# Kernel tuning notes

Hardware: AMD Instinct MI355X
Metric: run time of the kernel (lower is better)

Reference implementation:

```python
import jax, jax.numpy as jnp
import numpy as np

NUM_HEADS = 12

def setup_inputs() -> dict:
    key = jax.random.key(0)
    ks = jax.random.split(key, 6)
    B, N, C, T = 1, 4096, 768, 16
    return {
        "x": jax.random.normal(ks[0], (B, N, C), dtype=jnp.float32),
        "templates": jax.random.normal(ks[1], (T, 3 * C, C), dtype=jnp.float32) * 0.02,
        "coeffs": jax.random.normal(ks[2], (2, T, 1), dtype=jnp.float32),
        "qkv_bias": jnp.zeros((3 * C,), dtype=jnp.float32),
        "proj_w": jax.random.normal(ks[3], (C, C), dtype=jnp.float32) * 0.02,
        "proj_b": jnp.zeros((C,), dtype=jnp.float32),
    }

def reference(x, templates, coeffs, qkv_bias, proj_w, proj_b):
    B, N, C = x.shape
    H = NUM_HEADS
    hd = C // H
    scale = hd ** -0.5
    # template bank: each of num_cf coefficient sets builds a (3C, C) weight; average them
    num_cf = coeffs.shape[0]
    qkv_w = jnp.einsum('kt,toi->oi', coeffs[:, :, 0], templates) / num_cf  # (3C, C)
    qkv = x @ qkv_w.T + qkv_bias                                          # (B, N, 3C)
    qkv = qkv.reshape(B, N, 3, H, hd).transpose(2, 0, 3, 1, 4)            # (3, B, H, N, hd)
    q, k, v = qkv[0], qkv[1], qkv[2]
    attn = jax.nn.softmax(jnp.einsum('bhnd,bhmd->bhnm', q, k) * scale, axis=-1)
    out = jnp.einsum('bhnm,bhmd->bhnd', attn, v)                          # (B, H, N, hd)
    out = out.transpose(0, 2, 1, 3).reshape(B, N, C)
    return out @ proj_w.T + proj_b
```

## Files before the change

kernel.cpp:

```cpp
#include <hip/hip_runtime.h>
#include <stdint.h>

#define N_SEQ 4096
#define C_DIM 768
#define HEADS 12
#define HD    64
#define OI    (2304*768)

typedef __attribute__((ext_vector_type(8))) short short8;
typedef __attribute__((ext_vector_type(4))) float f32x4;
typedef __attribute__((ext_vector_type(16))) float f32x16;

__device__ __forceinline__ short f2bf(float f) {
  union { float f; unsigned u; } v; v.f = f;
  unsigned r = v.u + 0x7FFF + ((v.u >> 16) & 1);
  return (short)(r >> 16);
}
__device__ __forceinline__ short f2bf_trunc(float f) {
  union { float f; unsigned u; } v; v.f = f;
  return (short)(v.u >> 16);
}

__global__ __launch_bounds__(256) void prep_qkvw(const float* __restrict__ tmpl,
                                                 const float* __restrict__ coeffs,
                                                 short* __restrict__ w_bf) {
  __shared__ float c[16];
  if (threadIdx.x < 16)
    c[threadIdx.x] = 0.5f * (coeffs[threadIdx.x] + coeffs[16 + threadIdx.x]);
  __syncthreads();
  int idx = blockIdx.x * 256 + threadIdx.x;
  int base = idx * 4;
  if (base >= OI) return;
  float ax = 0.f, ay = 0.f, az = 0.f, aw = 0.f;
#pragma unroll
  for (int t = 0; t < 16; ++t) {
    float4 v = *(const float4*)(tmpl + (size_t)t * OI + base);
    float ct = c[t];
    ax = fmaf(ct, v.x, ax); ay = fmaf(ct, v.y, ay);
    az = fmaf(ct, v.z, az); aw = fmaf(ct, v.w, aw);
  }
  short4 o = make_short4(f2bf(ax), f2bf(ay), f2bf(az), f2bf(aw));
  *(short4*)(w_bf + base) = o;
}

__global__ __launch_bounds__(256) void cvt_bf16(const float* __restrict__ src,
                                                short* __restrict__ dst, int n4) {
  int i = blockIdx.x * 256 + threadIdx.x;
  if (i >= n4) return;
  float4 v = ((const float4*)src)[i];
  ((short4*)dst)[i] = make_short4(f2bf(v.x), f2bf(v.y), f2bf(v.z), f2bf(v.w));
}

#define GST 40
#define QSCALE 0.1803368801111204f
__global__ __launch_bounds__(256) void gemm_qkv(const short* __restrict__ A,
                                                const short* __restrict__ B,
                                                const float* __restrict__ bias,
                                                short* __restrict__ qkv_out) {
  __shared__ short As[128 * GST];
  __shared__ short Bs[128 * GST];
  int tid = threadIdx.x;
  int wave = tid >> 6, lane = tid & 63, g = lane >> 4, l15 = lane & 15;
  int wm = (wave >> 1) * 64, wn = (wave & 1) * 64;
  size_t mblk = (size_t)blockIdx.x * 128;
  size_t nblk = (size_t)blockIdx.y * 128;

  f32x4 acc[4][4];
#pragma unroll
  for (int mi = 0; mi < 4; ++mi)
#pragma unroll
    for (int ni = 0; ni < 4; ++ni)
#pragma unroll
      for (int r = 0; r < 4; ++r) acc[mi][ni][r] = 0.f;

  int row0 = tid >> 2;
  int c8   = (tid & 3) * 8;

  for (int k0 = 0; k0 < 768; k0 += 32) {
    short8 a0 = *(const short8*)(A + (mblk + row0) * 768 + k0 + c8);
    short8 a1 = *(const short8*)(A + (mblk + row0 + 64) * 768 + k0 + c8);
    short8 b0 = *(const short8*)(B + (nblk + row0) * 768 + k0 + c8);
    short8 b1 = *(const short8*)(B + (nblk + row0 + 64) * 768 + k0 + c8);
    __syncthreads();
    *(short8*)(As + row0 * GST + c8) = a0;
    *(short8*)(As + (row0 + 64) * GST + c8) = a1;
    *(short8*)(Bs + row0 * GST + c8) = b0;
    *(short8*)(Bs + (row0 + 64) * GST + c8) = b1;
    __syncthreads();
    short8 af[4], bfr[4];
#pragma unroll
    for (int mi = 0; mi < 4; ++mi)
      af[mi] = *(const short8*)(As + (wm + mi * 16 + l15) * GST + g * 8);
#pragma unroll
    for (int ni = 0; ni < 4; ++ni)
      bfr[ni] = *(const short8*)(Bs + (wn + ni * 16 + l15) * GST + g * 8);
#pragma unroll
    for (int mi = 0; mi < 4; ++mi)
#pragma unroll
      for (int ni = 0; ni < 4; ++ni)
        acc[mi][ni] = __builtin_amdgcn_mfma_f32_16x16x32_bf16(af[mi], bfr[ni], acc[mi][ni], 0, 0, 0);
  }

#pragma unroll
  for (int ni = 0; ni < 4; ++ni) {
    int col = (int)nblk + wn + ni * 16 + l15;
    int which = col / 768;
    int rem = col - which * 768;
    int h = rem >> 6, d = rem & 63;
    float bcol = bias[col];
    if (which == 2) {
      short* vbase = qkv_out + (size_t)2 * HEADS * N_SEQ * HD
                   + ((size_t)h * HD + d) * N_SEQ;
#pragma unroll
      for (int mi = 0; mi < 4; ++mi) {
        int rowb = (int)mblk + wm + mi * 16 + g * 4;
        short4 o;
        o.x = f2bf(acc[mi][ni][0] + bcol);
        o.y = f2bf(acc[mi][ni][1] + bcol);
        o.z = f2bf(acc[mi][ni][2] + bcol);
        o.w = f2bf(acc[mi][ni][3] + bcol);
        *(short4*)(vbase + rowb) = o;
      }
    } else {
      float sc = (which == 0) ? QSCALE : 1.0f;
      short* dst = qkv_out + ((size_t)which * HEADS + h) * N_SEQ * HD + d;
#pragma unroll
      for (int mi = 0; mi < 4; ++mi) {
        int rowb = (int)mblk + wm + mi * 16 + g * 4;
#pragma unroll
        for (int r = 0; r < 4; ++r)
          dst[(size_t)(rowb + r) * HD] = f2bf((acc[mi][ni][r] + bcol) * sc);
      }
    }
  }
}

__global__ __launch_bounds__(256) void gemm_proj(const short* __restrict__ A,
                                                 const short* __restrict__ B,
                                                 const float* __restrict__ bias,
                                                 float* __restrict__ C) {
  __shared__ short As[64 * GST];
  __shared__ short Bs[64 * GST];
  int tid = threadIdx.x;
  int wave = tid >> 6, lane = tid & 63, g = lane >> 4, l15 = lane & 15;
  int wm = (wave >> 1) * 32, wn = (wave & 1) * 32;
  size_t mblk = (size_t)blockIdx.x * 64;
  size_t nblk = (size_t)blockIdx.y * 64;

  f32x4 acc[2][2];
#pragma unroll
  for (int mi = 0; mi < 2; ++mi)
#pragma unroll
    for (int ni = 0; ni < 2; ++ni)
#pragma unroll
      for (int r = 0; r < 4; ++r) acc[mi][ni][r] = 0.f;

  int row0 = tid >> 2;
  int c8   = (tid & 3) * 8;

  for (int k0 = 0; k0 < 768; k0 += 32) {
    short8 a0 = *(const short8*)(A + (mblk + row0) * 768 + k0 + c8);
    short8 b0 = *(const short8*)(B + (nblk + row0) * 768 + k0 + c8);
    __syncthreads();
    *(short8*)(As + row0 * GST + c8) = a0;
    *(short8*)(Bs + row0 * GST + c8) = b0;
    __syncthreads();
    short8 af[2], bfr[2];
#pragma unroll
    for (int mi = 0; mi < 2; ++mi)
      af[mi] = *(const short8*)(As + (wm + mi * 16 + l15) * GST + g * 8);
#pragma unroll
    for (int ni = 0; ni < 2; ++ni)
      bfr[ni] = *(const short8*)(Bs + (wn + ni * 16 + l15) * GST + g * 8);
#pragma unroll
    for (int mi = 0; mi < 2; ++mi)
#pragma unroll
      for (int ni = 0; ni < 2; ++ni)
        acc[mi][ni] = __builtin_amdgcn_mfma_f32_16x16x32_bf16(af[mi], bfr[ni], acc[mi][ni], 0, 0, 0);
  }

#pragma unroll
  for (int ni = 0; ni < 2; ++ni) {
    int col = (int)nblk + wn + ni * 16 + l15;
    float bcol = bias[col];
#pragma unroll
    for (int mi = 0; mi < 2; ++mi) {
      int rowb = (int)mblk + wm + mi * 16 + g * 4;
#pragma unroll
      for (int r = 0; r < 4; ++r)
        C[(size_t)(rowb + r) * 768 + col] = acc[mi][ni][r] + bcol;
    }
  }
}

#define PST 68
__global__ __launch_bounds__(128) void attn_fa(const short* __restrict__ qkv_buf,
                                               short* __restrict__ out_bf) {
  __shared__ short Ks[64 * PST];
  __shared__ short Vt[64 * PST];
  __shared__ short Ps[2 * 32 * PST];
  __shared__ float ls[64];
  int h = blockIdx.y;
  int q0 = blockIdx.x * 64;
  int tid = threadIdx.x, wave = tid >> 6, lane = tid & 63;
  int q5 = lane & 31, h5 = lane >> 5;
  const short* qh  = qkv_buf + (size_t)(0 * HEADS + h) * N_SEQ * HD;
  const short* kh  = qkv_buf + (size_t)(1 * HEADS + h) * N_SEQ * HD;
  const short* vth = qkv_buf + (size_t)2 * HEADS * N_SEQ * HD + (size_t)h * HD * N_SEQ;

  short8 qf[4];
#pragma unroll
  for (int c = 0; c < 4; ++c)
    qf[c] = *(const short8*)(qh + (size_t)(q0 + wave * 32 + q5) * HD + c * 16 + h5 * 8);

  f32x16 o_acc[2];
#pragma unroll
  for (int dt = 0; dt < 2; ++dt)
#pragma unroll
    for (int r = 0; r < 16; ++r) o_acc[dt][r] = 0.f;
  float l_r = 0.f;

  int srow = tid >> 1;
  int shalf = (tid & 1) * 32;

  short8 kr[4], vr[4];
#pragma unroll
  for (int i = 0; i < 4; ++i) {
    kr[i] = *(const short8*)(kh + (size_t)srow * HD + shalf + 8 * i);
    vr[i] = *(const short8*)(vth + (size_t)srow * N_SEQ + shalf + 8 * i);
  }

  short* pw = Ps + wave * 32 * PST;

  for (int t0 = 0; t0 < N_SEQ; t0 += 64) {
    __syncthreads();
#pragma unroll
    for (int i = 0; i < 4; ++i) {
      *(short8*)(Ks + srow * PST + shalf + 8 * i) = kr[i];
      *(short8*)(Vt + srow * PST + shalf + 8 * i) = vr[i];
    }
    __syncthreads();

    if (t0 + 64 < N_SEQ) {
      int t1 = t0 + 64;
#pragma unroll
      for (int i = 0; i < 4; ++i) {
        kr[i] = *(const short8*)(kh + (size_t)(t1 + srow) * HD + shalf + 8 * i);
        vr[i] = *(const short8*)(vth + (size_t)srow * N_SEQ + t1 + shalf + 8 * i);
      }
    }

    f32x16 st[2];
#pragma unroll
    for (int kt = 0; kt < 2; ++kt)
#pragma unroll
      for (int r = 0; r < 16; ++r) st[kt][r] = 0.f;
#pragma unroll
    for (int c = 0; c < 4; ++c)
#pragma unroll
      for (int kt = 0; kt < 2; ++kt) {
        short8 kf = *(const short8*)(Ks + (kt * 32 + q5) * PST + c * 16 + h5 * 8);
        st[kt] = __builtin_amdgcn_mfma_f32_32x32x16_bf16(kf, qf[c], st[kt], 0, 0, 0);
      }

#pragma unroll
    for (int kt = 0; kt < 2; ++kt)
#pragma unroll
      for (int cc = 0; cc < 4; ++cc) {
        float p0 = __builtin_amdgcn_exp2f(st[kt][cc * 4 + 0]);
        float p1 = __builtin_amdgcn_exp2f(st[kt][cc * 4 + 1]);
        float p2 = __builtin_amdgcn_exp2f(st[kt][cc * 4 + 2]);
        float p3 = __builtin_amdgcn_exp2f(st[kt][cc * 4 + 3]);
        l_r += (p0 + p1) + (p2 + p3);
        short4 o = make_short4(f2bf_trunc(p0), f2bf_trunc(p1), f2bf_trunc(p2), f2bf_trunc(p3));
        *(short4*)(pw + q5 * PST + kt * 32 + cc * 8 + h5 * 4) = o;
      }

#pragma unroll
    for (int c = 0; c < 4; ++c) {
      short8 pf = *(const short8*)(pw + q5 * PST + c * 16 + h5 * 8);
#pragma unroll
      for (int dt = 0; dt < 2; ++dt) {
        short8 vf = *(const short8*)(Vt + (dt * 32 + q5) * PST + c * 16 + h5 * 8);
        o_acc[dt] = __builtin_amdgcn_mfma_f32_32x32x16_bf16(pf, vf, o_acc[dt], 0, 0, 0);
      }
    }
  }

  l_r += __shfl_xor(l_r, 32);
  if (h5 == 0) ls[wave * 32 + q5] = 1.0f / l_r;
  __syncthreads();

#pragma unroll
  for (int cc = 0; cc < 4; ++cc)
#pragma unroll
    for (int rr = 0; rr < 4; ++rr) {
      int qloc = rr + 8 * cc + 4 * h5;
      float inv = ls[wave * 32 + qloc];
      int qrow = q0 + wave * 32 + qloc;
#pragma unroll
      for (int dt = 0; dt < 2; ++dt)
        out_bf[(size_t)qrow * C_DIM + h * HD + dt * 32 + q5] =
            f2bf(o_acc[dt][cc * 4 + rr] * inv);
    }
}

extern "C" void kernel_launch(void* const* d_in, const int* in_sizes, int n_in,
                              void* d_out, int out_size, void* d_ws, size_t ws_size,
                              hipStream_t stream) {
  const float* x        = (const float*)d_in[0];
  const float* tmpl     = (const float*)d_in[1];
  const float* coeffs   = (const float*)d_in[2];
  const float* qkv_bias = (const float*)d_in[3];
  const float* proj_w   = (const float*)d_in[4];
  const float* proj_b   = (const float*)d_in[5];
  float* out = (float*)d_out;
  char* ws = (char*)d_ws;

  short* w_bf    = (short*)(ws);
  short* x_bf    = (short*)(ws + 3538944);
  short* pw_bf   = (short*)(ws + 9830400);
  short* qkvb    = (short*)(ws + 11010048);
  short* attn_bf = (short*)(ws + 29884416);

  prep_qkvw<<<1728, 256, 0, stream>>>(tmpl, coeffs, w_bf);
  cvt_bf16<<<3072, 256, 0, stream>>>(x, x_bf, 786432);
  cvt_bf16<<<576, 256, 0, stream>>>(proj_w, pw_bf, 147456);

  dim3 g1(32, 18);
  gemm_qkv<<<g1, 256, 0, stream>>>(x_bf, w_bf, qkv_bias, qkvb);

  dim3 ga(64, 12);
  attn_fa<<<ga, 128, 0, stream>>>(qkvb, attn_bf);

  dim3 g2(64, 12);
  gemm_proj<<<g2, 256, 0, stream>>>(attn_bf, pw_bf, proj_b, out);
}
```

Before: 349.3 us.

## Split attention KV range in two with partial outputs and a reduce kernel

Attention now splits each head's key range into two halves, doubling the grid to 1536 blocks, with a swizzled block index to spread heads across XCDs. Each half writes unnormalized fp32 partial outputs and row sums, and a new reduce kernel combines them, normalizes and converts to bf16. K fragments are now read straight from global memory instead of being staged in LDS, and launch bounds request higher occupancy. The cost is extra fp32 partial traffic, one more launch, and uncached-by-LDS K loads; the output buffer is reused as scratch for one partial.

New measurement: 372.1 us. +6.5%, slower.

```diff
diff --git a/kernel.cpp b/kernel.cpp
--- a/kernel.cpp
+++ b/kernel.cpp
@@ -194,16 +194,22 @@
 }
 
 #define PST 68
-__global__ __launch_bounds__(128) void attn_fa(const short* __restrict__ qkv_buf,
-                                               short* __restrict__ out_bf) {
-  __shared__ short Ks[64 * PST];
+__global__ __launch_bounds__(128, 3) void attn_fa(const short* __restrict__ qkv_buf,
+                                                  float* __restrict__ op0,
+                                                  float* __restrict__ op1,
+                                                  float* __restrict__ lp) {
   __shared__ short Vt[64 * PST];
   __shared__ short Ps[2 * 32 * PST];
-  __shared__ float ls[64];
-  int h = blockIdx.y;
-  int q0 = blockIdx.x * 64;
+  int bid = blockIdx.x;
+  int j = (bid & 7) * 192 + (bid >> 3);
+  int h = j >> 7;
+  int rj = j & 127;
+  int half = rj >> 6;
+  int qt = rj & 63;
   int tid = threadIdx.x, wave = tid >> 6, lane = tid & 63;
   int q5 = lane & 31, h5 = lane >> 5;
+  int q0 = qt * 64 + wave * 32;
+  int kvb = half * 2048;
   const short* qh  = qkv_buf + (size_t)(0 * HEADS + h) * N_SEQ * HD;
   const short* kh  = qkv_buf + (size_t)(1 * HEADS + h) * N_SEQ * HD;
   const short* vth = qkv_buf + (size_t)2 * HEADS * N_SEQ * HD + (size_t)h * HD * N_SEQ;
@@ -211,7 +217,7 @@
   short8 qf[4];
 #pragma unroll
   for (int c = 0; c < 4; ++c)
-    qf[c] = *(const short8*)(qh + (size_t)(q0 + wave * 32 + q5) * HD + c * 16 + h5 * 8);
+    qf[c] = *(const short8*)(qh + (size_t)(q0 + q5) * HD + c * 16 + h5 * 8);
 
   f32x16 o_acc[2];
 #pragma unroll
@@ -223,31 +229,24 @@
   int srow = tid >> 1;
   int shalf = (tid & 1) * 32;
 
-  short8 kr[4], vr[4];
-#pragma unroll
-  for (int i = 0; i < 4; ++i) {
-    kr[i] = *(const short8*)(kh + (size_t)srow * HD + shalf + 8 * i);
-    vr[i] = *(const short8*)(vth + (size_t)srow * N_SEQ + shalf + 8 * i);
-  }
+  short8 vr[4];
+#pragma unroll
+  for (int i = 0; i < 4; ++i)
+    vr[i] = *(const short8*)(vth + (size_t)srow * N_SEQ + kvb + shalf + 8 * i);
 
   short* pw = Ps + wave * 32 * PST;
 
-  for (int t0 = 0; t0 < N_SEQ; t0 += 64) {
-    __syncthreads();
-#pragma unroll
-    for (int i = 0; i < 4; ++i) {
-      *(short8*)(Ks + srow * PST + shalf + 8 * i) = kr[i];
+  for (int t0 = kvb; t0 < kvb + 2048; t0 += 64) {
+    __syncthreads();
+#pragma unroll
+    for (int i = 0; i < 4; ++i)
       *(short8*)(Vt + srow * PST + shalf + 8 * i) = vr[i];
-    }
-    __syncthreads();
-
-    if (t0 + 64 < N_SEQ) {
-      int t1 = t0 + 64;
-#pragma unroll
-      for (int i = 0; i < 4; ++i) {
-        kr[i] = *(const short8*)(kh + (size_t)(t1 + srow) * HD + shalf + 8 * i);
-        vr[i] = *(const short8*)(vth + (size_t)srow * N_SEQ + t1 + shalf + 8 * i);
-      }
+    __syncthreads();
+
+    if (t0 + 64 < kvb + 2048) {
+#pragma unroll
+      for (int i = 0; i < 4; ++i)
+        vr[i] = *(const short8*)(vth + (size_t)srow * N_SEQ + (t0 + 64) + shalf + 8 * i);
     }
 
     f32x16 st[2];
@@ -259,7 +258,7 @@
     for (int c = 0; c < 4; ++c)
 #pragma unroll
       for (int kt = 0; kt < 2; ++kt) {
-        short8 kf = *(const short8*)(Ks + (kt * 32 + q5) * PST + c * 16 + h5 * 8);
+        short8 kf = *(const short8*)(kh + (size_t)(t0 + kt * 32 + q5) * HD + c * 16 + h5 * 8);
         st[kt] = __builtin_amdgcn_mfma_f32_32x32x16_bf16(kf, qf[c], st[kt], 0, 0, 0);
       }
 
@@ -288,21 +287,38 @@
   }
 
   l_r += __shfl_xor(l_r, 32);
-  if (h5 == 0) ls[wave * 32 + q5] = 1.0f / l_r;
-  __syncthreads();
-
+
+  float* op = half ? op1 : op0;
 #pragma unroll
   for (int cc = 0; cc < 4; ++cc)
 #pragma unroll
     for (int rr = 0; rr < 4; ++rr) {
       int qloc = rr + 8 * cc + 4 * h5;
-      float inv = ls[wave * 32 + qloc];
-      int qrow = q0 + wave * 32 + qloc;
+      size_t base = ((size_t)h * N_SEQ + q0 + qloc) * HD;
 #pragma unroll
       for (int dt = 0; dt < 2; ++dt)
-        out_bf[(size_t)qrow * C_DIM + h * HD + dt * 32 + q5] =
-            f2bf(o_acc[dt][cc * 4 + rr] * inv);
-    }
+        op[base + dt * 32 + q5] = o_acc[dt][cc * 4 + rr];
+    }
+  if (h5 == 0)
+    lp[((size_t)half * HEADS + h) * N_SEQ + q0 + q5] = l_r;
+}
+
+__global__ __launch_bounds__(256) void attn_reduce(const float* __restrict__ op0,
+                                                   const float* __restrict__ op1,
+                                                   const float* __restrict__ lp,
+                                                   short* __restrict__ out_bf) {
+  int idx = blockIdx.x * 256 + threadIdx.x;
+  int d4 = idx & 15;
+  int n  = (idx >> 4) & 4095;
+  int h  = idx >> 16;
+  size_t o = ((size_t)h * N_SEQ + n) * HD + d4 * 4;
+  float4 a = *(const float4*)(op0 + o);
+  float4 b = *(const float4*)(op1 + o);
+  float l = lp[(size_t)h * N_SEQ + n] + lp[((size_t)HEADS + h) * N_SEQ + n];
+  float inv = 1.0f / l;
+  short4 s = make_short4(f2bf((a.x + b.x) * inv), f2bf((a.y + b.y) * inv),
+                         f2bf((a.z + b.z) * inv), f2bf((a.w + b.w) * inv));
+  *(short4*)(out_bf + (size_t)n * C_DIM + h * HD + d4 * 4) = s;
 }
 
 extern "C" void kernel_launch(void* const* d_in, const int* in_sizes, int n_in,
@@ -322,6 +338,9 @@
   short* pw_bf   = (short*)(ws + 9830400);
   short* qkvb    = (short*)(ws + 11010048);
   short* attn_bf = (short*)(ws + 29884416);
+  float* opart1  = (float*)(ws + 36175872);
+  float* lpart   = (float*)(ws + 48758784);
+  float* opart0  = out;
 
   prep_qkvw<<<1728, 256, 0, stream>>>(tmpl, coeffs, w_bf);
   cvt_bf16<<<3072, 256, 0, stream>>>(x, x_bf, 786432);
@@ -330,8 +349,8 @@
   dim3 g1(32, 18);
   gemm_qkv<<<g1, 256, 0, stream>>>(x_bf, w_bf, qkv_bias, qkvb);
 
-  dim3 ga(64, 12);
-  attn_fa<<<ga, 128, 0, stream>>>(qkvb, attn_bf);
+  attn_fa<<<1536, 128, 0, stream>>>(qkvb, opart0, opart1, lpart);
+  attn_reduce<<<3072, 256, 0, stream>>>(opart0, opart1, lpart, attn_bf);
 
   dim3 g2(64, 12);
   gemm_proj<<<g2, 256, 0, stream>>>(attn_bf, pw_bf, proj_b, out);
```
